# Kernel tuning notes

Hardware: AMD Instinct MI355X
Metric: run time of the kernel (lower is better)

The kernel has to match this reference:

```python
import jax, jax.numpy as jnp
import numpy as np

NUM_HEADS = 16
EPS = 1e-6

def _rms_norm(t, gamma):
    # t: (L,B,H,Dh), gamma: (Dh,)
    var = jnp.mean(t * t, axis=-1, keepdims=True)
    return t * jax.lax.rsqrt(var + EPS) * gamma

def _rotate_half(t):
    t1, t2 = jnp.split(t, 2, axis=-1)
    return jnp.concatenate([-t2, t1], axis=-1)

def _apply_rope(t, cos, sin):
    # t: (L,B,H,Dh); cos/sin: (L,1,1,Dh)
    return t * cos + _rotate_half(t) * sin

def setup_inputs() -> dict:
    key = jax.random.key(0)
    ks = jax.random.split(key, 8)
    T, H, W, B, D = 8, 20, 30, 1, 1024
    Dh = D // NUM_HEADS
    L = T * H * W
    x = jax.random.normal(ks[0], (T, H, W, B, D), dtype=jnp.float32)
    rope_emb = jax.random.normal(ks[1], (L, 1, 1, Dh), dtype=jnp.float32)  # angles
    s = 0.02
    wq = jax.random.normal(ks[2], (D, D), dtype=jnp.float32) * s
    wk = jax.random.normal(ks[3], (D, D), dtype=jnp.float32) * s
    wv = jax.random.normal(ks[4], (D, D), dtype=jnp.float32) * s
    wo = jax.random.normal(ks[5], (D, D), dtype=jnp.float32) * s
    q_gamma = jnp.ones((Dh,), dtype=jnp.float32)
    k_gamma = jnp.ones((Dh,), dtype=jnp.float32)
    return {"x": x, "rope_emb": rope_emb, "wq": wq, "wk": wk, "wv": wv,
            "wo": wo, "q_gamma": q_gamma, "k_gamma": k_gamma}

def reference(x, rope_emb, wq, wk, wv, wo, q_gamma, k_gamma):
    T, H, W, B, D = x.shape
    Hn = NUM_HEADS
    Dh = D // Hn
    L = T * H * W
    xs = x.reshape(L, B, D)  # sbhd token layout: (THW, B, D)
    # QKV projections (no bias), split into heads
    q = (xs @ wq.T).reshape(L, B, Hn, Dh)
    k = (xs @ wk.T).reshape(L, B, Hn, Dh)
    v = (xs @ wv.T).reshape(L, B, Hn, Dh)
    # per-head RMSNorm on Q and K ('RRI'), identity on V
    q = _rms_norm(q, q_gamma)
    k = _rms_norm(k, k_gamma)
    # rotary embedding on Q and K
    cos = jnp.cos(rope_emb)
    sin = jnp.sin(rope_emb)
    q = _apply_rope(q, cos, sin)
    k = _apply_rope(k, cos, sin)
    # scaled dot-product attention
    scale = 1.0 / jnp.sqrt(jnp.asarray(Dh, dtype=x.dtype))
    scores = jnp.einsum('lbhd,mbhd->bhlm', q, k) * scale  # (B,H,L,L)
    attn = jax.nn.softmax(scores, axis=-1)
    out = jnp.einsum('bhlm,mbhd->lbhd', attn, v).reshape(L, B, D)
    out = out @ wo.T
    return out.reshape(T, H, W, B, D)
```

## Files before the change

### kernel.cpp

```cpp
#include <hip/hip_runtime.h>

typedef __attribute__((ext_vector_type(4)))  float    f32x4;
typedef __attribute__((ext_vector_type(16))) float    f32x16;
typedef __attribute__((ext_vector_type(8)))  short    bf16x8;
typedef __attribute__((ext_vector_type(8)))  _Float16 f16x8;
typedef __attribute__((ext_vector_type(4)))  _Float16 f16x4;
typedef __attribute__((ext_vector_type(4)))  unsigned uint4v;
typedef __fp16 h2 __attribute__((ext_vector_type(2)));

__device__ inline unsigned pkrtz(float a, float b) {
    auto v = __builtin_amdgcn_cvt_pkrtz(a, b);
    return __builtin_bit_cast(unsigned, v);
}
__device__ inline float fexp2(float x) {
#if __has_builtin(__builtin_amdgcn_exp2f)
    return __builtin_amdgcn_exp2f(x);
#else
    return exp2f(x);
#endif
}
__device__ inline void gld16(void* lds, const void* g) {
    __builtin_amdgcn_global_load_lds(
        (const __attribute__((address_space(1))) void*)g,
        (__attribute__((address_space(3))) void*)lds, 16, 0, 0);
}

__device__ inline void half_exchange(unsigned& a0, unsigned& a1,
                                     unsigned& b0, unsigned& b1, int g2) {
#if __has_builtin(__builtin_amdgcn_permlane32_swap)
    {
        auto p = __builtin_amdgcn_permlane32_swap(a0, b0, false, false);
        a0 = p[0]; b0 = p[1];
        auto q = __builtin_amdgcn_permlane32_swap(a1, b1, false, false);
        a1 = q[0]; b1 = q[1];
    }
#else
    unsigned s0 = g2 ? a0 : b0, s1 = g2 ? a1 : b1;
    unsigned r0 = (unsigned)__shfl_xor((int)s0, 32);
    unsigned r1 = (unsigned)__shfl_xor((int)s1, 32);
    unsigned w0 = g2 ? r0 : a0, w1 = g2 ? r1 : a1;
    unsigned w2 = g2 ? b0 : r0, w3 = g2 ? b1 : r1;
    a0 = w0; a1 = w1; b0 = w2; b1 = w3;
#endif
}

__global__ __launch_bounds__(256) void split_all(
    const float* __restrict__ x,  const float* __restrict__ wq,
    const float* __restrict__ wk, const float* __restrict__ wv,
    const float* __restrict__ wo,
    _Float16* __restrict__ Xf, _Float16* __restrict__ Wqkvf,
    _Float16* __restrict__ Wof)
{
    const int b = blockIdx.x;
    const float* s; _Float16* d; int i;
    if (b < 2400)      { s = x;  d = Xf;                  i = b * 256 + threadIdx.x; }
    else if (b < 2912) { s = wq; d = Wqkvf;               i = (b - 2400) * 256 + threadIdx.x; }
    else if (b < 3424) { s = wk; d = Wqkvf + 1024 * 1024; i = (b - 2912) * 256 + threadIdx.x; }
    else if (b < 3936) { s = wv; d = Wqkvf + 2048 * 1024; i = (b - 3424) * 256 + threadIdx.x; }
    else               { s = wo; d = Wof;                 i = (b - 3936) * 256 + threadIdx.x; }

    f32x4 a = ((const f32x4*)s)[2 * i];
    f32x4 c = ((const f32x4*)s)[2 * i + 1];
    f16x8 v;
#pragma unroll
    for (int j = 0; j < 4; j++) { v[j] = (_Float16)a[j]; v[4 + j] = (_Float16)c[j]; }
    ((f16x8*)d)[i] = v;
}

__global__ __launch_bounds__(256) void gemm_qkv(
    const _Float16* __restrict__ Af, const _Float16* __restrict__ Bf,
    const float* __restrict__ rope,
    const float* __restrict__ qgam, const float* __restrict__ kgam,
    _Float16* __restrict__ Qh, _Float16* __restrict__ Kh,
    _Float16* __restrict__ Vt)
{
    __shared__ _Float16 sA[128 * 64], sB[128 * 64];

    const int tid = threadIdx.x, lane = tid & 63, wv = tid >> 6;
    const int wm = wv >> 1, wn = wv & 1;
    const int r = lane & 15, g = lane >> 4;
    const int lid = (blockIdx.x & 7) * 114 + (blockIdx.x >> 3);
    const int m0 = (lid / 24) * 128, n0 = (lid % 24) * 128;
    const int K = 1024, L = 4800;

    int srow[4], scol[4];
#pragma unroll
    for (int p = 0; p < 4; p++) {
        int c = tid + 256 * p;
        srow[p] = c >> 3;
        scol[p] = ((c & 7) ^ (srow[p] & 7)) * 8;
    }

    f32x4 acc[4][4];
#pragma unroll
    for (int mf = 0; mf < 4; mf++)
#pragma unroll
        for (int nf = 0; nf < 4; nf++)
            acc[mf][nf] = (f32x4){0.f, 0.f, 0.f, 0.f};

    for (int kk = 0; kk < K; kk += 64) {
        __syncthreads();
#pragma unroll
        for (int p = 0; p < 4; p++) {
            const int db = (tid + 256 * p) * 16;
            gld16((char*)sA + db, Af + (size_t)(m0 + srow[p]) * K + kk + scol[p]);
            gld16((char*)sB + db, Bf + (size_t)(n0 + srow[p]) * K + kk + scol[p]);
        }
        __syncthreads();

        f16x8 fb[4][2];
#pragma unroll
        for (int nf = 0; nf < 4; nf++) {
            int row = wn * 64 + nf * 16 + r;
#pragma unroll
            for (int kc = 0; kc < 2; kc++)
                fb[nf][kc] = *(const f16x8*)((const char*)sB + row * 128 + (((kc * 4 + g) ^ (row & 7)) * 16));
        }
#pragma unroll
        for (int mf = 0; mf < 4; mf++) {
            int row = wm * 64 + mf * 16 + r;
            f16x8 fa0 = *(const f16x8*)((const char*)sA + row * 128 + (((g) ^ (row & 7)) * 16));
            f16x8 fa1 = *(const f16x8*)((const char*)sA + row * 128 + (((4 + g) ^ (row & 7)) * 16));
#pragma unroll
            for (int nf = 0; nf < 4; nf++) {
                acc[mf][nf] = __builtin_amdgcn_mfma_f32_16x16x32_f16(fa0, fb[nf][0], acc[mf][nf], 0, 0, 0);
                acc[mf][nf] = __builtin_amdgcn_mfma_f32_16x16x32_f16(fa1, fb[nf][1], acc[mf][nf], 0, 0, 0);
            }
        }
    }

    const int col0  = n0 + wn * 64;
    const int which = col0 >> 10;
    const int hd    = (col0 & 1023) >> 6;

    if (which == 2) {
#pragma unroll
        for (int mf = 0; mf < 4; mf++) {
            const int l0 = m0 + wm * 64 + mf * 16 + 4 * g;
            if (l0 < L) {
#pragma unroll
                for (int nf = 0; nf < 4; nf++) {
                    f16x4 v4;
#pragma unroll
                    for (int e = 0; e < 4; e++) v4[e] = (_Float16)acc[mf][nf][e];
                    *(f16x4*)(Vt + (size_t)(hd * 64 + nf * 16 + r) * L + l0) = v4;
                }
            }
        }
        return;
    }

    const float* G = which ? kgam : qgam;
    const float qs = which ? 1.0f : 0.18033688011112042f;
    float gam[4];
#pragma unroll
    for (int nf = 0; nf < 4; nf++) gam[nf] = G[nf * 16 + r];
    _Float16* dst = which ? Kh : Qh;

#pragma unroll
    for (int mf = 0; mf < 4; mf++) {
        float ss[4];
#pragma unroll
        for (int e = 0; e < 4; e++)
            ss[e] = acc[mf][0][e] * acc[mf][0][e] + acc[mf][1][e] * acc[mf][1][e]
                  + acc[mf][2][e] * acc[mf][2][e] + acc[mf][3][e] * acc[mf][3][e];
#pragma unroll
        for (int mask = 1; mask < 16; mask <<= 1)
#pragma unroll
            for (int e = 0; e < 4; e++)
                ss[e] += __shfl_xor(ss[e], mask);
        float inv[4];
#pragma unroll
        for (int e = 0; e < 4; e++) inv[e] = rsqrtf(ss[e] * (1.0f / 64.0f) + 1e-6f);

        float xn[4][4];
#pragma unroll
        for (int nf = 0; nf < 4; nf++)
#pragma unroll
            for (int e = 0; e < 4; e++)
                xn[nf][e] = acc[mf][nf][e] * inv[e] * gam[nf];

#pragma unroll
        for (int e = 0; e < 4; e++) {
            const int l = m0 + wm * 64 + mf * 16 + 4 * g + e;
            if (l < L) {
#pragma unroll
                for (int nf = 0; nf < 4; nf++) {
                    float ang = rope[(size_t)l * 64 + nf * 16 + r];
                    float sv, cv;
                    __sincosf(ang, &sv, &cv);
                    float rot = (nf < 2) ? -xn[nf + 2][e] : xn[nf - 2][e];
                    dst[(size_t)l * 1024 + hd * 64 + nf * 16 + r] =
                        (_Float16)((xn[nf][e] * cv + rot * sv) * qs);
                }
            } else if (which == 0) {
#pragma unroll
                for (int nf = 0; nf < 4; nf++)
                    dst[(size_t)l * 1024 + hd * 64 + nf * 16 + r] = (_Float16)0.f;
            }
        }
    }
}

__global__ __launch_bounds__(256) void gemm_out_f16(
    const _Float16* __restrict__ Af, const _Float16* __restrict__ Bf,
    float* __restrict__ C)
{
    __shared__ _Float16 sA[64 * 32], sB[128 * 32];

    const int tid = threadIdx.x, lane = tid & 63, wv = tid >> 6;
    const int wm = wv >> 1, wn = wv & 1;
    const int r = lane & 15, g = lane >> 4;
    const int lid = (blockIdx.x & 7) * 75 + (blockIdx.x >> 3);
    const int m0 = (lid >> 3) * 64, n0 = (lid & 7) * 128;
    const int K = 1024;

    const int aar = tid >> 2, aac = ((tid & 3) ^ (aar & 3)) * 8;
    const size_t offA = (size_t)(m0 + aar) * K + aac;
    const int c0 = tid, c1 = tid + 256;
    const int br0 = c0 >> 2, bc0 = ((c0 & 3) ^ (br0 & 3)) * 8;
    const int br1 = c1 >> 2, bc1 = ((c1 & 3) ^ (br1 & 3)) * 8;
    const size_t offB0 = (size_t)(n0 + br0) * K + bc0;
    const size_t offB1 = (size_t)(n0 + br1) * K + bc1;
    const int dA = tid * 16, dB0 = tid * 16, dB1 = (tid + 256) * 16;

    f32x4 acc[2][4];
#pragma unroll
    for (int mf = 0; mf < 2; mf++)
#pragma unroll
        for (int nf = 0; nf < 4; nf++)
            acc[mf][nf] = (f32x4){0.f, 0.f, 0.f, 0.f};

    for (int kk = 0; kk < K; kk += 32) {
        __syncthreads();
        gld16((char*)sA + dA,  Af + offA + kk);
        gld16((char*)sB + dB0, Bf + offB0 + kk);
        gld16((char*)sB + dB1, Bf + offB1 + kk);
        __syncthreads();

        f16x8 fb[4];
#pragma unroll
        for (int nf = 0; nf < 4; nf++) {
            int row = wn * 64 + nf * 16 + r;
            fb[nf] = *(const f16x8*)((const char*)sB + row * 64 + ((g ^ (row & 3)) * 16));
        }
#pragma unroll
        for (int mf = 0; mf < 2; mf++) {
            int row = wm * 32 + mf * 16 + r;
            f16x8 fa = *(const f16x8*)((const char*)sA + row * 64 + ((g ^ (row & 3)) * 16));
#pragma unroll
            for (int nf = 0; nf < 4; nf++)
                acc[mf][nf] = __builtin_amdgcn_mfma_f32_16x16x32_f16(fa, fb[nf], acc[mf][nf], 0, 0, 0);
        }
    }

#pragma unroll
    for (int mf = 0; mf < 2; mf++)
#pragma unroll
        for (int nf = 0; nf < 4; nf++)
#pragma unroll
            for (int e = 0; e < 4; e++) {
                int row = m0 + wm * 32 + mf * 16 + 4 * g + e;
                int col = n0 + wn * 64 + nf * 16 + r;
                C[(size_t)row * 1024 + col] = acc[mf][nf][e];
            }
}

__global__ __launch_bounds__(256) void flash11(
    const _Float16* __restrict__ Qh, const _Float16* __restrict__ Kh,
    const _Float16* __restrict__ Vt,
    _Float16* __restrict__ Oph, float* __restrict__ Lp, int L)
{
    __shared__ _Float16 KT[2][4096];
    __shared__ _Float16 VT[2][4096];

    const int tid = threadIdx.x, lane = tid & 63, wv = tid >> 6;
    const int r = lane & 31, g2 = lane >> 5;

    const int li  = blockIdx.x >> 3;
    const int w   = (blockIdx.x & 7) * 152 + li;
    const int h   = w / 76;
    const int rem = w % 76;
    const int s   = rem / 38;
    const int qt  = rem % 38;
    const int q0  = qt * 128 + wv * 32;
    const int t0  = s * 38;
    const int nt  = s ? 37 : 38;

    f16x8 qf[4];
#pragma unroll
    for (int kc = 0; kc < 4; kc++)
        qf[kc] = *(const f16x8*)(Qh + (size_t)(q0 + r) * 1024 + h * 64 + kc * 16 + g2 * 8);

    int loff[2][4];
#pragma unroll
    for (int blk = 0; blk < 2; blk++)
#pragma unroll
        for (int kc = 0; kc < 4; kc++)
            loff[blk][kc] = (blk * 32 + r) * 128 + (((2 * kc + g2) ^ (r & 7)) * 16);

    const int p0c = tid, p1c = 256 + tid;
    const int sr0 = p0c >> 3, sc0 = (p0c & 7) ^ (sr0 & 7);
    const int sr1 = p1c >> 3, sc1 = (p1c & 7) ^ (sr1 & 7);
    const _Float16* ksrc0 = Kh + (size_t)(t0 * 64 + sr0) * 1024 + h * 64 + sc0 * 8;
    const _Float16* ksrc1 = Kh + (size_t)(t0 * 64 + sr1) * 1024 + h * 64 + sc1 * 8;
    const _Float16* vsrc0 = Vt + (size_t)(h * 64 + sr0) * L + t0 * 64 + sc0 * 8;
    const _Float16* vsrc1 = Vt + (size_t)(h * 64 + sr1) * L + t0 * 64 + sc1 * 8;

#define STAGE(buf) do { \
        gld16((char*)&KT[buf][0] + wv * 1024,        ksrc0); \
        gld16((char*)&KT[buf][0] + 4096 + wv * 1024, ksrc1); \
        gld16((char*)&VT[buf][0] + wv * 1024,        vsrc0); \
        gld16((char*)&VT[buf][0] + 4096 + wv * 1024, vsrc1); \
        ksrc0 += 64 * 1024; ksrc1 += 64 * 1024; vsrc0 += 64; vsrc1 += 64; \
    } while (0)

    f32x16 o[2];
#pragma unroll
    for (int nb = 0; nb < 2; nb++)
#pragma unroll
        for (int e = 0; e < 16; e++) o[nb][e] = 0.f;
    float lsum0 = 0.f, lsum1 = 0.f;

    f32x16 z16;
#pragma unroll
    for (int e = 0; e < 16; e++) z16[e] = 0.f;
    const h2 ones2 = {(__fp16)1.0f, (__fp16)1.0f};

    STAGE(0);
    __syncthreads();

#define TILE(buf, dostage) do { \
        if (dostage) STAGE(buf ^ 1); \
        f32x16 sc_[2]; \
        __builtin_amdgcn_s_setprio(1); \
        _Pragma("unroll") \
        for (int mk = 0; mk < 2; mk++) { \
            f16x8 kf0 = *(const f16x8*)((const char*)&KT[buf][0] + loff[mk][0]); \
            sc_[mk] = __builtin_amdgcn_mfma_f32_32x32x16_f16(kf0, qf[0], z16, 0, 0, 0); \
            _Pragma("unroll") \
            for (int kc = 1; kc < 4; kc++) { \
                f16x8 kf = *(const f16x8*)((const char*)&KT[buf][0] + loff[mk][kc]); \
                sc_[mk] = __builtin_amdgcn_mfma_f32_32x32x16_f16(kf, qf[kc], sc_[mk], 0, 0, 0); \
            } \
        } \
        __builtin_amdgcn_s_setprio(0); \
        f16x8 pa[4]; \
        _Pragma("unroll") \
        for (int mk = 0; mk < 2; mk++) { \
            float ps[16]; \
            _Pragma("unroll") for (int e = 0; e < 16; e++) ps[e] = fexp2(sc_[mk][e]); \
            _Pragma("unroll") \
            for (int c = 0; c < 2; c++) { \
                unsigned a0 = pkrtz(ps[8 * c + 0], ps[8 * c + 1]); \
                unsigned a1 = pkrtz(ps[8 * c + 2], ps[8 * c + 3]); \
                unsigned b0 = pkrtz(ps[8 * c + 4], ps[8 * c + 5]); \
                unsigned b1 = pkrtz(ps[8 * c + 6], ps[8 * c + 7]); \
                half_exchange(a0, a1, b0, b1, g2); \
                lsum0 = __builtin_amdgcn_fdot2(__builtin_bit_cast(h2, a0), ones2, lsum0, false); \
                lsum0 = __builtin_amdgcn_fdot2(__builtin_bit_cast(h2, a1), ones2, lsum0, false); \
                lsum1 = __builtin_amdgcn_fdot2(__builtin_bit_cast(h2, b0), ones2, lsum1, false); \
                lsum1 = __builtin_amdgcn_fdot2(__builtin_bit_cast(h2, b1), ones2, lsum1, false); \
                uint4v fr = {a0, a1, b0, b1}; \
                pa[2 * mk + c] = __builtin_bit_cast(f16x8, fr); \
            } \
        } \
        __builtin_amdgcn_s_setprio(1); \
        _Pragma("unroll") \
        for (int nb = 0; nb < 2; nb++) \
            _Pragma("unroll") \
            for (int kc = 0; kc < 4; kc++) { \
                f16x8 vf = *(const f16x8*)((const char*)&VT[buf][0] + loff[nb][kc]); \
                o[nb] = __builtin_amdgcn_mfma_f32_32x32x16_f16(pa[kc], vf, o[nb], 0, 0, 0); \
            } \
        __builtin_amdgcn_s_setprio(0); \
        __syncthreads(); \
    } while (0)

    for (int t = 0; t + 2 < nt; t += 2) { TILE(0, true); TILE(1, true); }
    if (s) { TILE(0, false); }
    else   { TILE(0, true); TILE(1, false); }

#undef TILE
#undef STAGE

    float lsum = lsum0 + lsum1;
    lsum += __shfl_xor(lsum, 32);
    if (g2 == 0 && q0 + r < 4800)
        Lp[(size_t)(s * 4800 + q0 + r) * 16 + h] = lsum;
#pragma unroll
    for (int reg = 0; reg < 16; reg++) {
        const int qrow = (reg & 3) + 8 * (reg >> 2) + 4 * g2;
        const int qg = q0 + qrow;
        if (qg < 4800) {
#pragma unroll
            for (int nb = 0; nb < 2; nb++)
                Oph[(size_t)(s * 4800 + qg) * 1024 + h * 64 + nb * 32 + r] =
                    (_Float16)(o[nb][reg] * 0.015625f);
        }
    }
}

__global__ __launch_bounds__(256) void merge_f16(
    const _Float16* __restrict__ Oph, const float* __restrict__ Lp,
    _Float16* __restrict__ AOf)
{
    const int q = blockIdx.x, t = threadIdx.x;
    const int d = t * 4, hh = d >> 6;
    f16x4 a = *(const f16x4*)(Oph + (size_t)q * 1024 + d);
    f16x4 b = *(const f16x4*)(Oph + (size_t)(4800 + q) * 1024 + d);
    const float inv = 64.0f / (Lp[(size_t)q * 16 + hh] + Lp[(size_t)(4800 + q) * 16 + hh]);
    f16x4 v;
#pragma unroll
    for (int j = 0; j < 4; j++)
        v[j] = (_Float16)(((float)a[j] + (float)b[j]) * inv);
    *(f16x4*)(AOf + (size_t)q * 1024 + d) = v;
}

extern "C" void kernel_launch(void* const* d_in, const int* in_sizes, int n_in,
                              void* d_out, int out_size, void* d_ws, size_t ws_size,
                              hipStream_t stream)
{
    const float* x    = (const float*)d_in[0];
    const float* rope = (const float*)d_in[1];
    const float* wq   = (const float*)d_in[2];
    const float* wk   = (const float*)d_in[3];
    const float* wv   = (const float*)d_in[4];
    const float* wo   = (const float*)d_in[5];
    const float* qg   = (const float*)d_in[6];
    const float* kg   = (const float*)d_in[7];
    float* out = (float*)d_out;

    const int L = 4800;
    char* ws = (char*)d_ws;

    _Float16* Oph  = (_Float16*)ws;
    float* Lp      = (float*)(ws + 39321600);
    _Float16* Wof  = (_Float16*)(ws + 39936000);
    _Float16* Qh   = (_Float16*)(ws + 44130304);
    _Float16* Kh   = Qh + 4864 * 1024;
    _Float16* Vt   = Kh + 4800 * 1024;
    _Float16* Xf   = (_Float16*)(ws + 73752576);
    _Float16* Wqkvf= (_Float16*)(ws + 83582976);
    _Float16* AOf  = (_Float16*)(ws + 44130304);

    split_all<<<4448, 256, 0, stream>>>(x, wq, wk, wv, wo, Xf, Wqkvf, Wof);
    gemm_qkv<<<912, 256, 0, stream>>>(Xf, Wqkvf, rope, qg, kg, Qh, Kh, Vt);
    flash11<<<1216, 256, 0, stream>>>(Qh, Kh, Vt, Oph, Lp, L);
    merge_f16<<<4800, 256, 0, stream>>>(Oph, Lp, AOf);
    gemm_out_f16<<<600, 256, 0, stream>>>(AOf, Wof, out);
}
```

Before: 217.9 us.

## Fuse split-KV merge and normalization into output projection GEMM

Removes the separate merge kernel and instead has the output-projection GEMM load both partial attention outputs, sum them, and scale by the per-head inverse softmax denominators computed into shared memory. This eliminates one kernel launch and the write and re-read of the merged activation buffer. In exchange, the GEMM now streams two A tiles per k-step and performs the add and scale in half precision rather than fp32, slightly increasing per-iteration work and rounding error.

New measurement: 221.1 us. Within noise of the previous version (+1.5%).

```diff
diff --git a/kernel.cpp b/kernel.cpp
--- a/kernel.cpp
+++ b/kernel.cpp
@@ -202,11 +202,12 @@
     }
 }
 
-__global__ __launch_bounds__(256) void gemm_out_f16(
-    const _Float16* __restrict__ Af, const _Float16* __restrict__ Bf,
-    float* __restrict__ C)
+__global__ __launch_bounds__(256) void gemm_out_fused(
+    const _Float16* __restrict__ Oph, const float* __restrict__ Lp,
+    const _Float16* __restrict__ Bf, float* __restrict__ C)
 {
-    __shared__ _Float16 sA[64 * 32], sB[128 * 32];
+    __shared__ _Float16 sA0[64 * 32], sA1[64 * 32], sB[128 * 32];
+    __shared__ float invT[64 * 17];
 
     const int tid = threadIdx.x, lane = tid & 63, wv = tid >> 6;
     const int wm = wv >> 1, wn = wv & 1;
@@ -215,8 +216,17 @@
     const int m0 = (lid >> 3) * 64, n0 = (lid & 7) * 128;
     const int K = 1024;
 
+#pragma unroll
+    for (int e = 0; e < 4; e++) {
+        const int idx = tid + 256 * e;
+        const int row = idx >> 4, hh = idx & 15;
+        invT[row * 17 + hh] = 64.0f /
+            (Lp[(size_t)(m0 + row) * 16 + hh] + Lp[(size_t)(4800 + m0 + row) * 16 + hh]);
+    }
+
     const int aar = tid >> 2, aac = ((tid & 3) ^ (aar & 3)) * 8;
-    const size_t offA = (size_t)(m0 + aar) * K + aac;
+    const size_t offA0 = (size_t)(m0 + aar) * K + aac;
+    const size_t offA1 = (size_t)(4800 + m0 + aar) * K + aac;
     const int c0 = tid, c1 = tid + 256;
     const int br0 = c0 >> 2, bc0 = ((c0 & 3) ^ (br0 & 3)) * 8;
     const int br1 = c1 >> 2, bc1 = ((c1 & 3) ^ (br1 & 3)) * 8;
@@ -233,11 +243,13 @@
 
     for (int kk = 0; kk < K; kk += 32) {
         __syncthreads();
-        gld16((char*)sA + dA,  Af + offA + kk);
-        gld16((char*)sB + dB0, Bf + offB0 + kk);
-        gld16((char*)sB + dB1, Bf + offB1 + kk);
+        gld16((char*)sA0 + dA,  Oph + offA0 + kk);
+        gld16((char*)sA1 + dA,  Oph + offA1 + kk);
+        gld16((char*)sB + dB0,  Bf + offB0 + kk);
+        gld16((char*)sB + dB1,  Bf + offB1 + kk);
         __syncthreads();
 
+        const int hh = kk >> 6;
         f16x8 fb[4];
 #pragma unroll
         for (int nf = 0; nf < 4; nf++) {
@@ -247,10 +259,15 @@
 #pragma unroll
         for (int mf = 0; mf < 2; mf++) {
             int row = wm * 32 + mf * 16 + r;
-            f16x8 fa = *(const f16x8*)((const char*)sA + row * 64 + ((g ^ (row & 3)) * 16));
+            int byt = row * 64 + ((g ^ (row & 3)) * 16);
+            f16x8 fa0 = *(const f16x8*)((const char*)sA0 + byt);
+            f16x8 fa1 = *(const f16x8*)((const char*)sA1 + byt);
+            const _Float16 sc = (_Float16)invT[row * 17 + hh];
+            f16x8 sv = {sc, sc, sc, sc, sc, sc, sc, sc};
+            f16x8 fs = (fa0 + fa1) * sv;
 #pragma unroll
             for (int nf = 0; nf < 4; nf++)
-                acc[mf][nf] = __builtin_amdgcn_mfma_f32_16x16x32_f16(fa, fb[nf], acc[mf][nf], 0, 0, 0);
+                acc[mf][nf] = __builtin_amdgcn_mfma_f32_16x16x32_f16(fs, fb[nf], acc[mf][nf], 0, 0, 0);
         }
     }
 
@@ -260,8 +277,8 @@
         for (int nf = 0; nf < 4; nf++)
 #pragma unroll
             for (int e = 0; e < 4; e++) {
-                int row = m0 + wm * 32 + mf * 16 + 4 * g + e;
-                int col = n0 + wn * 64 + nf * 16 + r;
+                const int row = m0 + wm * 32 + mf * 16 + 4 * g + e;
+                const int col = n0 + wn * 64 + nf * 16 + r;
                 C[(size_t)row * 1024 + col] = acc[mf][nf][e];
             }
 }
@@ -401,22 +418,6 @@
     }
 }
 
-__global__ __launch_bounds__(256) void merge_f16(
-    const _Float16* __restrict__ Oph, const float* __restrict__ Lp,
-    _Float16* __restrict__ AOf)
-{
-    const int q = blockIdx.x, t = threadIdx.x;
-    const int d = t * 4, hh = d >> 6;
-    f16x4 a = *(const f16x4*)(Oph + (size_t)q * 1024 + d);
-    f16x4 b = *(const f16x4*)(Oph + (size_t)(4800 + q) * 1024 + d);
-    const float inv = 64.0f / (Lp[(size_t)q * 16 + hh] + Lp[(size_t)(4800 + q) * 16 + hh]);
-    f16x4 v;
-#pragma unroll
-    for (int j = 0; j < 4; j++)
-        v[j] = (_Float16)(((float)a[j] + (float)b[j]) * inv);
-    *(f16x4*)(AOf + (size_t)q * 1024 + d) = v;
-}
-
 extern "C" void kernel_launch(void* const* d_in, const int* in_sizes, int n_in,
                               void* d_out, int out_size, void* d_ws, size_t ws_size,
                               hipStream_t stream)
@@ -442,11 +443,9 @@
     _Float16* Vt   = Kh + 4800 * 1024;
     _Float16* Xf   = (_Float16*)(ws + 73752576);
     _Float16* Wqkvf= (_Float16*)(ws + 83582976);
-    _Float16* AOf  = (_Float16*)(ws + 44130304);
 
     split_all<<<4448, 256, 0, stream>>>(x, wq, wk, wv, wo, Xf, Wqkvf, Wof);
     gemm_qkv<<<912, 256, 0, stream>>>(Xf, Wqkvf, rope, qg, kg, Qh, Kh, Vt);
     flash11<<<1216, 256, 0, stream>>>(Qh, Kh, Vt, Oph, Lp, L);
-    merge_f16<<<4800, 256, 0, stream>>>(Oph, Lp, AOf);
-    gemm_out_f16<<<600, 256, 0, stream>>>(AOf, Wof, out);
-}
+    gemm_out_fused<<<600, 256, 0, stream>>>(Oph, Lp, Wof, out);
+}
```
